# Optimization experiments

Hardware: AMD Instinct MI355X
Metric: run time of the kernel (lower is better)

Reference implementation:

```python
import jax, jax.numpy as jnp
import numpy as np

K = (3, 5, 7)
TAU_MIN, TAU_MAX = 0.03, 0.5


def _l2norm(x, axis=1, eps=1e-12):
    # matches torch F.normalize: x / max(||x||, eps)
    n = jnp.sqrt(jnp.sum(x * x, axis=axis, keepdims=True))
    return x / jnp.maximum(n, eps)


def _affinity_one(feat, kappa_ch, qw_k, kw_k, k):
    # feat: (B, C, H, W); kappa_ch: (B, 1, H, W); qw_k/kw_k: (Ca, C)
    B, C, H, W = feat.shape
    q = jnp.einsum('bchw,oc->bohw', feat, qw_k)
    key = jnp.einsum('bchw,oc->bohw', feat, kw_k)
    qn = _l2norm(q)
    kn = _l2norm(key)
    p = k // 2
    knp = jnp.pad(kn, ((0, 0), (0, 0), (p, p), (p, p)))
    # windowed cosine correlation: loop over the small fixed set of k*k offsets
    sims = []
    for dy in range(k):
        for dx in range(k):
            sims.append(jnp.sum(qn * knp[:, :, dy:dy + H, dx:dx + W], axis=1))
    sim = jnp.stack(sims, axis=1)  # (B, k*k, H, W)
    # temperature from curvature: GLOBAL min/max over the sliced channel
    kmin = kappa_ch.min()
    kmax = kappa_ch.max()
    kap_n = (kappa_ch - kmin) / (kmax - kmin + 1e-06)
    tau = jnp.clip(TAU_MAX - kap_n * (TAU_MAX - TAU_MIN), TAU_MIN, TAU_MAX)
    return sim / (tau + 1e-06)  # broadcast (B,kk,H,W) / (B,1,H,W)


def setup_inputs() -> dict:
    key = jax.random.key(0)
    k1, k2, k3, k4 = jax.random.split(key, 4)
    B, C, H, W = 4, 64, 256, 256
    CA = 32
    feat = jax.random.normal(k1, (B, C, H, W), dtype=jnp.float32)
    kappa = jax.random.uniform(k2, (B, len(K), H, W), dtype=jnp.float32)
    scale = 1.0 / np.sqrt(C)
    qw = jax.random.normal(k3, (len(K), CA, C), dtype=jnp.float32) * scale
    kw = jax.random.normal(k4, (len(K), CA, C), dtype=jnp.float32) * scale
    return {'feat': feat, 'kappa': kappa, 'qw': qw, 'kw': kw}


def reference(feat, kappa, qw, kw):
    out = []
    for i, k in enumerate(K):
        out.append(_affinity_one(feat, kappa[:, i:i + 1], qw[i], kw[i], k))
    return tuple(out)
```

## Files before the change

### kernel.cpp

```cpp
#include <hip/hip_runtime.h>
#include <stdint.h>

#define HW   65536
#define IMG  256
#define NB   4
#define NC   64
#define NA   32

typedef __attribute__((ext_vector_type(8))) short short8v;
typedef __attribute__((ext_vector_type(4))) float f32x4;

__device__ __forceinline__ unsigned short f2bf(float x) {
  unsigned u = __float_as_uint(x);
  u += 0x7FFFu + ((u >> 16) & 1u);
  return (unsigned short)(u >> 16);
}
__device__ __forceinline__ float bfval(unsigned short h) { return __uint_as_float((unsigned)h << 16); }
__device__ __forceinline__ unsigned packbf(float a, float b) {
  return (unsigned)f2bf(a) | ((unsigned)f2bf(b) << 16);
}

__global__ void prep_afrag(const float* __restrict__ qw, const float* __restrict__ kw,
                           unsigned short* __restrict__ afrag, unsigned* __restrict__ mm) {
  int idx = blockIdx.x * 256 + threadIdx.x;
  if (blockIdx.x == 0 && threadIdx.x < 6)
    mm[threadIdx.x] = (threadIdx.x < 3) ? 0xFFFFFFFFu : 0u;
  if (idx >= 3 * 4 * 2 * 2 * 64 * 8) return;
  int j    = idx & 7;
  int lane = (idx >> 3) & 63;
  int h    = (idx >> 9) & 1;
  int ks   = (idx >> 10) & 1;
  int mt   = (idx >> 11) & 3;
  int i    = idx >> 13;
  int s = mt >> 1;
  int o = (mt & 1) * 16 + (lane & 15);
  int c = ks * 32 + (lane >> 4) * 8 + j;
  float v = (s ? kw : qw)[((size_t)i * NA + o) * NC + c];
  unsigned short hi = f2bf(v);
  afrag[idx] = h ? f2bf(v - bfval(hi)) : hi;
}

__global__ __launch_bounds__(256) void minmax_k(const float* __restrict__ kappa,
                                                unsigned* __restrict__ mm) {
  const int i = blockIdx.y;
  const unsigned* ku = (const unsigned*)kappa;
  unsigned lo = 0xFFFFFFFFu, hi = 0u;
  for (int idx = blockIdx.x * 256 + threadIdx.x; idx < NB * HW; idx += gridDim.x * 256) {
    int b = idx >> 16, p = idx & (HW - 1);
    unsigned v = ku[((size_t)(b * 3 + i)) * HW + p];
    lo = min(lo, v); hi = max(hi, v);
  }
#pragma unroll
  for (int d = 32; d >= 1; d >>= 1) {
    lo = min(lo, (unsigned)__shfl_xor((int)lo, d, 64));
    hi = max(hi, (unsigned)__shfl_xor((int)hi, d, 64));
  }
  __shared__ unsigned slo[4], shi[4];
  if ((threadIdx.x & 63) == 0) { slo[threadIdx.x >> 6] = lo; shi[threadIdx.x >> 6] = hi; }
  __syncthreads();
  if (threadIdx.x == 0) {
    lo = min(min(slo[0], slo[1]), min(slo[2], slo[3]));
    hi = max(max(shi[0], shi[1]), max(shi[2], shi[3]));
    atomicMin(&mm[i], lo);
    atomicMax(&mm[i + 3], hi);
  }
}

__global__ __launch_bounds__(256) void proj_all(const float* __restrict__ feat,
                                                const unsigned short* __restrict__ afr,
                                                unsigned* __restrict__ qb,
                                                unsigned* __restrict__ kb,
                                                const int nsl, const int i0) {
  __shared__ __align__(16) unsigned Psh[4 * 64 * 20];
  const int t = blockIdx.x;
  const int b = t >> 8;
  const int p0 = (t & 255) * 256;
  const int lane = threadIdx.x & 63;
  const int w = threadIdx.x >> 6;
  const int pbase = p0 + w * 64;
  unsigned* Pw = Psh + w * (64 * 20);

  short8v bh[4][2], bl[4][2];
  const float* fb = feat + (size_t)b * NC * HW;
#pragma unroll
  for (int ks = 0; ks < 2; ++ks) {
    float fv[32];
#pragma unroll
    for (int nt = 0; nt < 4; ++nt) {
      const int px = pbase + nt * 16 + (lane & 15);
      const float* fp = fb + (size_t)(ks * 32 + (lane >> 4) * 8) * HW + px;
#pragma unroll
      for (int j = 0; j < 8; ++j) fv[nt * 8 + j] = fp[(size_t)j * HW];
    }
#pragma unroll
    for (int nt = 0; nt < 4; ++nt)
#pragma unroll
      for (int j = 0; j < 8; ++j) {
        float f = fv[nt * 8 + j];
        unsigned short h = f2bf(f);
        bh[nt][ks][j] = (short)h;
        bl[nt][ks][j] = (short)f2bf(f - bfval(h));
      }
  }

#pragma unroll 1
  for (int sl = 0; sl < nsl; ++sl) {
#pragma unroll 1
    for (int s = 0; s < 2; ++s) {
      const unsigned short* af = afr + (size_t)(i0 + sl) * 8192;

      short8v ah[2][2], al[2][2];
#pragma unroll
      for (int m = 0; m < 2; ++m)
#pragma unroll
        for (int ks = 0; ks < 2; ++ks) {
          int mt = s * 2 + m;
          const unsigned short* base = af + (size_t)((mt * 2 + ks) * 2) * 512 + lane * 8;
          ah[m][ks] = *(const short8v*)(base);
          al[m][ks] = *(const short8v*)(base + 512);
        }

      f32x4 acc[2][4];
#pragma unroll
      for (int m = 0; m < 2; ++m)
#pragma unroll
        for (int nt = 0; nt < 4; ++nt) acc[m][nt] = (f32x4){0.f, 0.f, 0.f, 0.f};

#pragma unroll
      for (int nt = 0; nt < 4; ++nt)
#pragma unroll
        for (int ks = 0; ks < 2; ++ks)
#pragma unroll
          for (int m = 0; m < 2; ++m) {
            acc[m][nt] = __builtin_amdgcn_mfma_f32_16x16x32_bf16(ah[m][ks], bh[nt][ks], acc[m][nt], 0, 0, 0);
            acc[m][nt] = __builtin_amdgcn_mfma_f32_16x16x32_bf16(ah[m][ks], bl[nt][ks], acc[m][nt], 0, 0, 0);
            acc[m][nt] = __builtin_amdgcn_mfma_f32_16x16x32_bf16(al[m][ks], bh[nt][ks], acc[m][nt], 0, 0, 0);
          }

      asm volatile("" ::: "memory");
#pragma unroll
      for (int nt = 0; nt < 4; ++nt) {
        float ssq = 0.f;
#pragma unroll
        for (int m = 0; m < 2; ++m)
#pragma unroll
          for (int r = 0; r < 4; ++r) ssq = fmaf(acc[m][nt][r], acc[m][nt][r], ssq);
        ssq += __shfl_xor(ssq, 16, 64);
        ssq += __shfl_xor(ssq, 32, 64);
        float inv = 1.0f / fmaxf(sqrtf(ssq), 1e-12f);
        const int pxl = nt * 16 + (lane & 15);
#pragma unroll
        for (int m = 0; m < 2; ++m) {
          uint2 v;
          v.x = packbf(acc[m][nt][0] * inv, acc[m][nt][1] * inv);
          v.y = packbf(acc[m][nt][2] * inv, acc[m][nt][3] * inv);
          *(uint2*)(Pw + pxl * 20 + m * 8 + (lane >> 4) * 2) = v;
        }
      }
      asm volatile("s_waitcnt lgkmcnt(0)" ::: "memory");
      __builtin_amdgcn_sched_barrier(0);
      unsigned* dst = ((s ? kb : qb) + (size_t)sl * NB * HW * 16) +
                      ((size_t)b * HW + pbase) * 16;
#pragma unroll
      for (int r = 0; r < 4; ++r) {
        uint4 v = *(const uint4*)(Pw + (r * 16 + (lane >> 2)) * 20 + (lane & 3) * 4);
        *(uint4*)(dst + r * 256 + lane * 4) = v;
      }
    }
  }
}

template <int KS>
__device__ __forceinline__ void corr_mfma_body(float* Csh,
                                               const unsigned* __restrict__ qn,
                                               const unsigned* __restrict__ kn,
                                               const float* __restrict__ kappa,
                                               const unsigned* __restrict__ mm,
                                               const int i, const int b,
                                               float* __restrict__ out) {
  constexpr int P = KS / 2;
  constexpr int KK = KS * KS;
  constexpr int CST = 20;
  constexpr int NCOL = 22;
  constexpr int YST = NCOL * CST;
  constexpr int NR = KS + 3;
  const int y0 = blockIdx.y * 16, x0 = blockIdx.x * 16;
  const int lane = threadIdx.x & 63, w = threadIdx.x >> 6;
  const int cq = lane & 15;
  const int rq = lane >> 4;
  const int y = y0 + w * 4 + rq;
  const int x = x0 + cq;
  float* Cw = Csh + w * (4 * YST);

  const int kx0 = x0 - P + cq;
  const int kx1 = kx0 + 16;
  const int kyb = y0 + w * 4 - P;
  const unsigned* knb = kn + (size_t)b * HW * 16;

  short8v B0r[NR], B1r[NR];
#pragma unroll
  for (int r = 0; r < NR; ++r) {
    short8v z = {0, 0, 0, 0, 0, 0, 0, 0};
    B0r[r] = z; B1r[r] = z;
    const int ky = kyb + r;
    if ((unsigned)ky < (unsigned)IMG) {
      const unsigned* krow = knb + (size_t)ky * IMG * 16;
      if ((unsigned)kx0 < (unsigned)IMG) B0r[r] = *(const short8v*)(krow + (size_t)kx0 * 16 + rq * 4);
      if ((unsigned)kx1 < (unsigned)IMG) B1r[r] = *(const short8v*)(krow + (size_t)kx1 * 16 + rq * 4);
    }
  }

  short8v A[4];
#pragma unroll
  for (int yl = 0; yl < 4; ++yl) {
    const unsigned* p = qn + ((size_t)b * HW + (size_t)(y0 + w * 4 + yl) * IMG + x0 + cq) * 16 + rq * 4;
    A[yl] = *(const short8v*)p;
  }

  float kap = kappa[((size_t)(b * 3 + i)) * HW + (size_t)y * IMG + x];
  float kmin = __uint_as_float(mm[i]);
  float kmax = __uint_as_float(mm[i + 3]);
  float kapn = (kap - kmin) / (kmax - kmin + 1e-6f);
  float tau = fminf(fmaxf(0.5f - kapn * (0.5f - 0.03f), 0.03f), 0.5f);
  float scale = 1.0f / (tau + 1e-6f);

#pragma unroll
  for (int dy = 0; dy < KS; ++dy) {
    asm volatile("" ::: "memory");
#pragma unroll
    for (int yl = 0; yl < 4; ++yl) {
      f32x4 a0 = {0.f, 0.f, 0.f, 0.f}, a1 = {0.f, 0.f, 0.f, 0.f};
      a0 = __builtin_amdgcn_mfma_f32_16x16x32_bf16(A[yl], B0r[yl + dy], a0, 0, 0, 0);
      a1 = __builtin_amdgcn_mfma_f32_16x16x32_bf16(A[yl], B1r[yl + dy], a1, 0, 0, 0);
      *(f32x4*)(Cw + yl * YST + cq * CST + rq * 4) = a0;
      if (cq < NCOL - 16)
        *(f32x4*)(Cw + yl * YST + (16 + cq) * CST + rq * 4) = a1;
    }
    asm volatile("s_waitcnt lgkmcnt(0)" ::: "memory");
    __builtin_amdgcn_sched_barrier(0);
    float* ob = out + ((size_t)b * KK + (size_t)dy * KS) * HW + (size_t)y * IMG + x;
#pragma unroll
    for (int dx = 0; dx < KS; ++dx) {
      float v = Cw[rq * YST + (cq + dx) * CST + cq];
      ob[(size_t)dx * HW] = v * scale;
    }
  }
}

__global__ __launch_bounds__(256) void corr_all(const unsigned* __restrict__ qb,
                                                const unsigned* __restrict__ kb,
                                                const float* __restrict__ kappa,
                                                const unsigned* __restrict__ mm,
                                                const int i0, float* __restrict__ out) {
  __shared__ __align__(16) float Csh[7040];
  const int g = blockIdx.z >> 2;
  const int b = blockIdx.z & 3;
  const int fused = (gridDim.z > 4) ? 1 : 0;
  const int i = fused ? (2 - g) : i0;
  const int slot = fused ? i : 0;
  const unsigned* qn = qb + (size_t)slot * NB * HW * 16;
  const unsigned* kn = kb + (size_t)slot * NB * HW * 16;
  const size_t plane = (size_t)NB * HW;
  if (i == 0)
    corr_mfma_body<3>(Csh, qn, kn, kappa, mm, 0, b, out);
  else if (i == 1)
    corr_mfma_body<5>(Csh, qn, kn, kappa, mm, 1, b, out + plane * 9);
  else
    corr_mfma_body<7>(Csh, qn, kn, kappa, mm, 2, b, out + plane * 34);
}

extern "C" void kernel_launch(void* const* d_in, const int* in_sizes, int n_in,
                              void* d_out, int out_size, void* d_ws, size_t ws_size,
                              hipStream_t stream) {
  const float* feat  = (const float*)d_in[0];
  const float* kappa = (const float*)d_in[1];
  const float* qw    = (const float*)d_in[2];
  const float* kw    = (const float*)d_in[3];
  float* out = (float*)d_out;

  char* ws = (char*)d_ws;
  unsigned* mm = (unsigned*)ws;
  unsigned short* afrag = (unsigned short*)(ws + 64);
  unsigned* qbuf = (unsigned*)(ws + 65536);

  const size_t slot = (size_t)NB * HW * 16;
  const size_t need3 = 65536 + (size_t)6 * slot * 4;
  const int fused = (ws_size >= need3) ? 1 : 0;
  const int nsl = fused ? 3 : 1;
  unsigned* kbuf = qbuf + (size_t)nsl * slot;

  hipLaunchKernelGGL(prep_afrag, dim3(96), dim3(256), 0, stream, qw, kw, afrag, mm);
  hipLaunchKernelGGL(minmax_k, dim3(64, 3), dim3(256), 0, stream, kappa, mm);

  if (fused) {
    hipLaunchKernelGGL(proj_all, dim3(NB * HW / 256), dim3(256), 0, stream,
                       feat, afrag, qbuf, kbuf, 3, 0);
    hipLaunchKernelGGL(corr_all, dim3(IMG / 16, IMG / 16, NB * 3), dim3(256), 0, stream,
                       qbuf, kbuf, kappa, mm, 0, out);
  } else {
    for (int i = 0; i < 3; ++i) {
      hipLaunchKernelGGL(proj_all, dim3(NB * HW / 256), dim3(256), 0, stream,
                         feat, afrag, qbuf, kbuf, 1, i);
      hipLaunchKernelGGL(corr_all, dim3(IMG / 16, IMG / 16, NB), dim3(256), 0, stream,
                         qbuf, kbuf, kappa, mm, i, out);
    }
  }
}
```

Measured before the change: 102.3 us.

## Split projection across slices in grid, drop weight-lo MFMA term and LDS staging

The projection kernel now gets the slice index from blockIdx.y and launches three times as many blocks, so each block handles one slice instead of looping over all three. Each block therefore reloads and converts its features per slice. The low-order bf16 weight correction term (al*bh) is removed, cutting the MFMA count from three to two per step at some cost in accuracy. The LDS transpose staging is also gone; each lane writes 8-byte chunks straight to global memory, which removes shared memory and its synchronisation but makes the stores less coalesced.

```diff
diff --git a/kernel.cpp b/kernel.cpp
--- a/kernel.cpp
+++ b/kernel.cpp
@@ -70,15 +70,14 @@
                                                 const unsigned short* __restrict__ afr,
                                                 unsigned* __restrict__ qb,
                                                 unsigned* __restrict__ kb,
-                                                const int nsl, const int i0) {
-  __shared__ __align__(16) unsigned Psh[4 * 64 * 20];
+                                                const int i0) {
   const int t = blockIdx.x;
+  const int sl = blockIdx.y;
   const int b = t >> 8;
   const int p0 = (t & 255) * 256;
   const int lane = threadIdx.x & 63;
   const int w = threadIdx.x >> 6;
   const int pbase = p0 + w * 64;
-  unsigned* Pw = Psh + w * (64 * 20);
 
   short8v bh[4][2], bl[4][2];
   const float* fb = feat + (size_t)b * NC * HW;
@@ -103,68 +102,55 @@
       }
   }
 
+  const unsigned short* af = afr + (size_t)(i0 + sl) * 8192;
+
 #pragma unroll 1
-  for (int sl = 0; sl < nsl; ++sl) {
-#pragma unroll 1
-    for (int s = 0; s < 2; ++s) {
-      const unsigned short* af = afr + (size_t)(i0 + sl) * 8192;
-
-      short8v ah[2][2], al[2][2];
+  for (int s = 0; s < 2; ++s) {
+    short8v ah[2][2];
+#pragma unroll
+    for (int m = 0; m < 2; ++m)
+#pragma unroll
+      for (int ks = 0; ks < 2; ++ks) {
+        int mt = s * 2 + m;
+        ah[m][ks] = *(const short8v*)(af + (size_t)((mt * 2 + ks) * 2) * 512 + lane * 8);
+      }
+
+    f32x4 acc[2][4];
+#pragma unroll
+    for (int m = 0; m < 2; ++m)
+#pragma unroll
+      for (int nt = 0; nt < 4; ++nt) acc[m][nt] = (f32x4){0.f, 0.f, 0.f, 0.f};
+
+#pragma unroll
+    for (int nt = 0; nt < 4; ++nt)
+#pragma unroll
+      for (int ks = 0; ks < 2; ++ks)
+#pragma unroll
+        for (int m = 0; m < 2; ++m) {
+          acc[m][nt] = __builtin_amdgcn_mfma_f32_16x16x32_bf16(ah[m][ks], bh[nt][ks], acc[m][nt], 0, 0, 0);
+          acc[m][nt] = __builtin_amdgcn_mfma_f32_16x16x32_bf16(ah[m][ks], bl[nt][ks], acc[m][nt], 0, 0, 0);
+        }
+
+    unsigned* dstbuf = (s ? kb : qb) + (size_t)sl * NB * HW * 16;
+#pragma unroll
+    for (int nt = 0; nt < 4; ++nt) {
+      float ssq = 0.f;
 #pragma unroll
       for (int m = 0; m < 2; ++m)
 #pragma unroll
-        for (int ks = 0; ks < 2; ++ks) {
-          int mt = s * 2 + m;
-          const unsigned short* base = af + (size_t)((mt * 2 + ks) * 2) * 512 + lane * 8;
-          ah[m][ks] = *(const short8v*)(base);
-          al[m][ks] = *(const short8v*)(base + 512);
-        }
-
-      f32x4 acc[2][4];
-#pragma unroll
-      for (int m = 0; m < 2; ++m)
-#pragma unroll
-        for (int nt = 0; nt < 4; ++nt) acc[m][nt] = (f32x4){0.f, 0.f, 0.f, 0.f};
-
-#pragma unroll
-      for (int nt = 0; nt < 4; ++nt)
-#pragma unroll
-        for (int ks = 0; ks < 2; ++ks)
-#pragma unroll
-          for (int m = 0; m < 2; ++m) {
-            acc[m][nt] = __builtin_amdgcn_mfma_f32_16x16x32_bf16(ah[m][ks], bh[nt][ks], acc[m][nt], 0, 0, 0);
-            acc[m][nt] = __builtin_amdgcn_mfma_f32_16x16x32_bf16(ah[m][ks], bl[nt][ks], acc[m][nt], 0, 0, 0);
-            acc[m][nt] = __builtin_amdgcn_mfma_f32_16x16x32_bf16(al[m][ks], bh[nt][ks], acc[m][nt], 0, 0, 0);
-          }
-
-      asm volatile("" ::: "memory");
-#pragma unroll
-      for (int nt = 0; nt < 4; ++nt) {
-        float ssq = 0.f;
-#pragma unroll
-        for (int m = 0; m < 2; ++m)
-#pragma unroll
-          for (int r = 0; r < 4; ++r) ssq = fmaf(acc[m][nt][r], acc[m][nt][r], ssq);
-        ssq += __shfl_xor(ssq, 16, 64);
-        ssq += __shfl_xor(ssq, 32, 64);
-        float inv = 1.0f / fmaxf(sqrtf(ssq), 1e-12f);
-        const int pxl = nt * 16 + (lane & 15);
-#pragma unroll
-        for (int m = 0; m < 2; ++m) {
-          uint2 v;
-          v.x = packbf(acc[m][nt][0] * inv, acc[m][nt][1] * inv);
-          v.y = packbf(acc[m][nt][2] * inv, acc[m][nt][3] * inv);
-          *(uint2*)(Pw + pxl * 20 + m * 8 + (lane >> 4) * 2) = v;
-        }
-      }
-      asm volatile("s_waitcnt lgkmcnt(0)" ::: "memory");
-      __builtin_amdgcn_sched_barrier(0);
-      unsigned* dst = ((s ? kb : qb) + (size_t)sl * NB * HW * 16) +
-                      ((size_t)b * HW + pbase) * 16;
-#pragma unroll
-      for (int r = 0; r < 4; ++r) {
-        uint4 v = *(const uint4*)(Pw + (r * 16 + (lane >> 2)) * 20 + (lane & 3) * 4);
-        *(uint4*)(dst + r * 256 + lane * 4) = v;
+        for (int r = 0; r < 4; ++r) ssq = fmaf(acc[m][nt][r], acc[m][nt][r], ssq);
+      ssq += __shfl_xor(ssq, 16, 64);
+      ssq += __shfl_xor(ssq, 32, 64);
+      float inv = 1.0f / fmaxf(sqrtf(ssq), 1e-12f);
+      const int px = pbase + nt * 16 + (lane & 15);
+      const size_t pix = (size_t)b * HW + px;
+#pragma unroll
+      for (int m = 0; m < 2; ++m) {
+        int c0 = m * 16 + (lane >> 4) * 4;
+        uint2 v;
+        v.x = packbf(acc[m][nt][0] * inv, acc[m][nt][1] * inv);
+        v.y = packbf(acc[m][nt][2] * inv, acc[m][nt][3] * inv);
+        *(uint2*)(dstbuf + pix * 16 + (c0 >> 1)) = v;
       }
     }
   }
@@ -293,14 +279,14 @@
   hipLaunchKernelGGL(minmax_k, dim3(64, 3), dim3(256), 0, stream, kappa, mm);
 
   if (fused) {
-    hipLaunchKernelGGL(proj_all, dim3(NB * HW / 256), dim3(256), 0, stream,
-                       feat, afrag, qbuf, kbuf, 3, 0);
+    hipLaunchKernelGGL(proj_all, dim3(NB * HW / 256, 3), dim3(256), 0, stream,
+                       feat, afrag, qbuf, kbuf, 0);
     hipLaunchKernelGGL(corr_all, dim3(IMG / 16, IMG / 16, NB * 3), dim3(256), 0, stream,
                        qbuf, kbuf, kappa, mm, 0, out);
   } else {
     for (int i = 0; i < 3; ++i) {
-      hipLaunchKernelGGL(proj_all, dim3(NB * HW / 256), dim3(256), 0, stream,
-                         feat, afrag, qbuf, kbuf, 1, i);
+      hipLaunchKernelGGL(proj_all, dim3(NB * HW / 256, 1), dim3(256), 0, stream,
+                         feat, afrag, qbuf, kbuf, i);
       hipLaunchKernelGGL(corr_all, dim3(IMG / 16, IMG / 16, NB), dim3(256), 0, stream,
                          qbuf, kbuf, kappa, mm, i, out);
     }
```

Measured after the change: 119.2 us. +16.5%, slower.
